# Kernel optimization log

Hardware: AMD Instinct MI355X
Metric: run time of the kernel (lower is better)

Reference implementation:

```python
import jax, jax.numpy as jnp
import numpy as np

EPS = 1e-8
TOP_K = 2


def _l2norm(v, axis=-1):
    # F.normalize: v / max(||v||_2, eps)
    n = jnp.sqrt(jnp.sum(v * v, axis=axis, keepdims=True))
    return v / jnp.maximum(n, EPS)


def setup_inputs() -> dict:
    key = jax.random.key(0)
    ks = jax.random.split(key, 5)
    B, S, D, F, E = 2, 2048, 512, 2048, 8
    x = jax.random.normal(ks[0], (B, S, D), dtype=jnp.float32)
    anchors = jax.random.normal(ks[1], (E, D), dtype=jnp.float32)
    W1 = jax.random.normal(ks[2], (E, D, F), dtype=jnp.float32) * (1.0 / np.sqrt(D))
    b1 = jnp.zeros((E, F), dtype=jnp.float32)
    W2 = jax.random.normal(ks[3], (E, F, D), dtype=jnp.float32) * (1.0 / np.sqrt(F))
    b2 = jnp.zeros((E, D), dtype=jnp.float32)
    return {"x": x, "anchors": anchors, "W1": W1, "b1": b1, "W2": W2, "b2": b2}


def reference(x, anchors, W1, b1, W2, b2):
    B, S, D = x.shape
    E = anchors.shape[0]
    x_flat = x.reshape(B * S, D)  # (T, D)

    # Semantic resonance routing: cosine similarity with anchors
    x_n = _l2norm(x_flat)
    a_n = _l2norm(anchors)
    scores = jnp.einsum('td,ed->te', x_n, a_n)  # (T, E)

    # Noisy top-k (eval mode: no noise) + softmax gates over top-k scores
    topk_scores, topk_idx = jax.lax.top_k(scores, TOP_K)  # (T, K)
    gates = jax.nn.softmax(topk_scores, axis=-1)  # (T, K)

    # Combine weights per (token, expert); top-k indices are distinct per token
    T = B * S
    combine = jnp.zeros((T, E), dtype=x.dtype)
    combine = combine.at[jnp.arange(T)[:, None], topk_idx].add(gates)

    # Per-expert MLP (Linear -> exact GELU -> Linear), combined by gates.
    # Dense-over-experts form is mathematically identical to the sorted
    # grouped dispatch + index_add in the original module.
    h = jnp.einsum('td,edf->tef', x_flat, W1) + b1[None]  # (T, E, F)
    h = jax.nn.gelu(h, approximate=False)
    y = jnp.einsum('tef,efd->ted', h, W2) + b2[None]  # (T, E, D)
    out_flat = jnp.einsum('te,ted->td', combine, y)  # (T, D)

    out = out_flat.reshape(B, S, D)
    # aux_data equivalents: anchors_norm, resonance_scores, topk_indices
    return out, a_n, scores, topk_idx
```

## Files before the change

### kernel.cpp

```cpp
#include <hip/hip_runtime.h>
#include <cstdint>


#define T_TOK 4096
#define D_DIM 512
#define F_DIM 2048
#define E_EXP 8
#define NROWS 9216
#define MAXTILES 72

typedef __bf16 bf16x8 __attribute__((ext_vector_type(8)));
typedef float  f32x4  __attribute__((ext_vector_type(4)));
typedef unsigned short u16;

__device__ __forceinline__ u16 f2b(float f) {
    return __builtin_bit_cast(unsigned short, (__bf16)f);
}
__device__ __forceinline__ void gload16(void* lds, const void* g) {
    __builtin_amdgcn_global_load_lds(
        (const __attribute__((address_space(1))) void*)g,
        (__attribute__((address_space(3))) void*)lds, 16, 0, 0);
}

__global__ void anchors_k(const float* __restrict__ anchors,
                          float* __restrict__ an, float* __restrict__ dout_an) {
    int tid = threadIdx.x;
    int lane = tid & 63, e = tid >> 6;
    const float4* ar = (const float4*)(anchors + e * D_DIM + lane * 8);
    float4 v0 = ar[0], v1 = ar[1];
    float ss = v0.x*v0.x + v0.y*v0.y + v0.z*v0.z + v0.w*v0.w
             + v1.x*v1.x + v1.y*v1.y + v1.z*v1.z + v1.w*v1.w;
#pragma unroll
    for (int off = 32; off >= 1; off >>= 1) ss += __shfl_xor(ss, off, 64);
    float inv = 1.0f / fmaxf(sqrtf(ss), 1e-8f);
    float o[8] = {v0.x*inv, v0.y*inv, v0.z*inv, v0.w*inv,
                  v1.x*inv, v1.y*inv, v1.z*inv, v1.w*inv};
#pragma unroll
    for (int i = 0; i < 8; ++i) {
        an[e * D_DIM + lane * 8 + i] = o[i];
        dout_an[e * D_DIM + lane * 8 + i] = o[i];
    }
}

__global__ void routing_k(const float* __restrict__ x, const float* __restrict__ an,
                          float* __restrict__ dout_scores, float* __restrict__ dout_idx,
                          int* __restrict__ idxs, float* __restrict__ gates,
                          int* __restrict__ cnt) {
    __shared__ float anl[E_EXP * 544];
    __shared__ int hist[E_EXP];
    int tid = threadIdx.x;
    if (tid < E_EXP) hist[tid] = 0;
    for (int i = tid; i < E_EXP * D_DIM; i += 256) {
        int e = i >> 9, d = i & 511;
        anl[e * 544 + (d >> 7) * 136 + (d & 127)] = an[i];
    }
    __syncthreads();

    int p = tid & 3;
    int tok = blockIdx.x * 64 + (tid >> 2);
    const float4* xr = (const float4*)(x + (size_t)tok * D_DIM + p * 128);
    const float* ab = &anl[p * 136];
    float dot[E_EXP] = {};
    float ss = 0.f;
    for (int c = 0; c < 32; ++c) {
        float4 xv = xr[c];
        ss += xv.x*xv.x + xv.y*xv.y + xv.z*xv.z + xv.w*xv.w;
#pragma unroll
        for (int e = 0; e < E_EXP; ++e) {
            float4 av = *(const float4*)&ab[e * 544 + c * 4];
            dot[e] += xv.x*av.x + xv.y*av.y + xv.z*av.z + xv.w*av.w;
        }
    }
#pragma unroll
    for (int off = 1; off <= 2; off <<= 1) {
        ss += __shfl_xor(ss, off, 64);
#pragma unroll
        for (int e = 0; e < E_EXP; ++e) dot[e] += __shfl_xor(dot[e], off, 64);
    }

    if (p == 0) {
        float inv = 1.0f / fmaxf(sqrtf(ss), 1e-8f);
        float s[E_EXP];
#pragma unroll
        for (int e = 0; e < E_EXP; ++e) s[e] = dot[e] * inv;
        int i0 = 0; float b0 = s[0];
#pragma unroll
        for (int e = 1; e < E_EXP; ++e) if (s[e] > b0) { b0 = s[e]; i0 = e; }
        int i1 = -1; float b1v = -1e30f;
#pragma unroll
        for (int e = 0; e < E_EXP; ++e)
            if (e != i0 && s[e] > b1v) { b1v = s[e]; i1 = e; }
        if (i1 < 0) { i1 = (i0 + 1) & 7; b1v = s[i1]; }
        float g0 = 1.0f / (1.0f + expf(b1v - b0));
        float g1 = 1.0f - g0;
#pragma unroll
        for (int e = 0; e < E_EXP; ++e) dout_scores[tok * E_EXP + e] = s[e];
        dout_idx[tok * 2 + 0] = (float)i0;
        dout_idx[tok * 2 + 1] = (float)i1;
        idxs[tok * 2 + 0] = i0; idxs[tok * 2 + 1] = i1;
        gates[tok * 2 + 0] = g0; gates[tok * 2 + 1] = g1;
        atomicAdd(&hist[i0], 1);
        atomicAdd(&hist[i1], 1);
    }
    __syncthreads();
    if (tid < E_EXP) atomicAdd(&cnt[tid], hist[tid]);
}

__global__ void offs_k(const int* __restrict__ cnt, int* __restrict__ offs,
                       int* __restrict__ cur) {
    if (threadIdx.x == 0 && blockIdx.x == 0) {
        int acc = 0;
        for (int e = 0; e < E_EXP; ++e) {
            offs[e] = acc; cur[e] = acc;
            acc += (cnt[e] + 127) & ~127;
        }
        offs[E_EXP] = acc;
    }
}

__global__ void assign_k(const int* __restrict__ idxs, const float* __restrict__ gates,
                         int* __restrict__ cur, int* __restrict__ rowmap,
                         float* __restrict__ rowgate) {
    int t = blockIdx.x * 256 + threadIdx.x;
    if (t >= T_TOK) return;
#pragma unroll
    for (int k = 0; k < 2; ++k) {
        int e = idxs[t * 2 + k];
        e = min(max(e, 0), E_EXP - 1);
        int r = atomicAdd(&cur[e], 1);
        if (r >= 0 && r < NROWS) {
            rowmap[r] = t;
            rowgate[r] = gates[t * 2 + k];
        }
    }
}

__global__ void gather_k(const float* __restrict__ x, const int* __restrict__ rowmap,
                         u16* __restrict__ Xg) {
    int r = blockIdx.x;
    int t = rowmap[r];
    int c = threadIdx.x * 2;
    ushort2 o;
    if (t < 0 || t >= T_TOK) { o.x = 0; o.y = 0; }
    else {
        float2 v = *(const float2*)(x + (size_t)t * D_DIM + c);
        o.x = f2b(v.x); o.y = f2b(v.y);
    }
    *(ushort2*)(Xg + (size_t)r * D_DIM + c) = o;
}

__global__ void transpose_cast_k(const float* __restrict__ in, u16* __restrict__ out,
                                 int R, int C) {
    size_t zoff = (size_t)blockIdx.z * R * C;
    in += zoff; out += zoff;
    __shared__ float t[32][33];
    int c0 = blockIdx.x * 32, r0 = blockIdx.y * 32;
    int tx = threadIdx.x, ty = threadIdx.y;
#pragma unroll
    for (int j = 0; j < 32; j += 8)
        t[ty + j][tx] = in[(size_t)(r0 + ty + j) * C + c0 + tx];
    __syncthreads();
#pragma unroll
    for (int j = 0; j < 32; j += 8)
        out[(size_t)(c0 + ty + j) * R + r0 + tx] = f2b(t[tx][ty + j]);
}

template <int MODE>
__launch_bounds__(256, 2)
__global__ void gemm_k(const u16* __restrict__ A, int lda,
                       const u16* __restrict__ BtBase, int ldb,
                       u16* __restrict__ Hout, const float* __restrict__ b1,
                       float* __restrict__ outacc,
                       const int* __restrict__ rowmap, const float* __restrict__ rowgate,
                       const int* __restrict__ offs, int kPer) {
    int row0 = blockIdx.y * 128;
    if (row0 >= offs[E_EXP]) return;
    int e = 0;
#pragma unroll
    for (int i = 1; i < E_EXP; ++i) if (row0 >= offs[i]) e = i;
    const u16* Bt = BtBase + (size_t)e * D_DIM * F_DIM;
    int n0 = blockIdx.x * 128;
    int k_begin = (MODE == 1) ? (int)blockIdx.z * kPer : 0;
    int k_end = k_begin + kPer;

    alignas(16) __shared__ u16 As[128 * 64];
    alignas(16) __shared__ u16 Bs[128 * 64];

    int tid = threadIdx.x;
    int lane = tid & 63;
    int wv = tid >> 6;
    int wm = wv & 1, wn = wv >> 1;
    int kq = lane >> 4;
    int l15 = lane & 15;

    const u16* aSrc[4]; const u16* bSrc[4];
    u16* aDst[4]; u16* bDst[4];
#pragma unroll
    for (int i = 0; i < 4; ++i) {
        int slot = i * 256 + tid;
        int m = slot >> 3;
        int kc = slot & 7;
        aSrc[i] = A + (size_t)(row0 + m) * lda + kc * 8;
        bSrc[i] = Bt + (size_t)(n0 + m) * ldb + kc * 8;
        aDst[i] = As + slot * 8;
        bDst[i] = Bs + slot * 8;
    }

    f32x4 acc[4][4];
#pragma unroll
    for (int i = 0; i < 4; ++i)
#pragma unroll
        for (int j = 0; j < 4; ++j) acc[i][j] = f32x4{0.f, 0.f, 0.f, 0.f};

    for (int k0 = k_begin; k0 < k_end; k0 += 64) {
#pragma unroll
        for (int i = 0; i < 4; ++i) gload16(aDst[i], aSrc[i] + k0);
#pragma unroll
        for (int i = 0; i < 4; ++i) gload16(bDst[i], bSrc[i] + k0);
        asm volatile("s_waitcnt vmcnt(0)" ::: "memory");
        __syncthreads();
#pragma unroll
        for (int kk = 0; kk < 2; ++kk) {
            int kc = kk * 4 + kq;
            bf16x8 af[4], bfr[4];
#pragma unroll
            for (int i = 0; i < 4; ++i) {
                int rowA = wm * 64 + i * 16 + l15;
                af[i] = *(const bf16x8*)(As + rowA * 64 + kc * 8);
                int rowB = wn * 64 + i * 16 + l15;
                bfr[i] = *(const bf16x8*)(Bs + rowB * 64 + kc * 8);
            }
#pragma unroll
            for (int i = 0; i < 4; ++i)
#pragma unroll
                for (int j = 0; j < 4; ++j)
                    acc[i][j] = __builtin_amdgcn_mfma_f32_16x16x32_bf16(
                        af[i], bfr[j], acc[i][j], 0, 0, 0);
        }
        __syncthreads();
    }

    if constexpr (MODE == 0) {
        const float* b1e = b1 + (size_t)e * F_DIM;
#pragma unroll
        for (int i = 0; i < 4; ++i) {
            int gr = row0 + wm * 64 + i * 16 + kq * 4;
#pragma unroll
            for (int j = 0; j < 4; ++j) {
                int gc = n0 + wn * 64 + j * 16 + l15;
                float bb = b1e[gc];
#pragma unroll
                for (int r = 0; r < 4; ++r) {
                    float v = acc[i][j][r] + bb;
                    float h = 0.5f * v * (1.0f + erff(v * 0.70710678118f));
                    Hout[(size_t)(gr + r) * F_DIM + gc] = f2b(h);
                }
            }
        }
    } else {
#pragma unroll
        for (int i = 0; i < 4; ++i) {
            int grb = row0 + wm * 64 + i * 16 + kq * 4;
#pragma unroll
            for (int r = 0; r < 4; ++r) {
                int tok = rowmap[grb + r];
                float g = rowgate[grb + r];
                if (tok >= 0 && tok < T_TOK) {
                    float* orow = outacc + (size_t)tok * D_DIM;
#pragma unroll
                    for (int j = 0; j < 4; ++j) {
                        int gc = n0 + wn * 64 + j * 16 + l15;
                        atomicAdd(orow + gc, g * acc[i][j][r]);
                    }
                }
            }
        }
    }
}

__global__ void final_k(const float* __restrict__ outacc, const int* __restrict__ idxs,
                        const float* __restrict__ gates, const float* __restrict__ b2,
                        float* __restrict__ dout) {
    int t = blockIdx.x;
    int i0 = min(max(idxs[t * 2], 0), E_EXP - 1);
    int i1 = min(max(idxs[t * 2 + 1], 0), E_EXP - 1);
    float g0 = gates[t * 2], g1 = gates[t * 2 + 1];
    int d = threadIdx.x * 2;
    float2 oa = *(const float2*)(outacc + (size_t)t * D_DIM + d);
    const float* p0 = b2 + (size_t)i0 * D_DIM + d;
    const float* p1 = b2 + (size_t)i1 * D_DIM + d;
    float2 o;
    o.x = oa.x + g0 * p0[0] + g1 * p1[0];
    o.y = oa.y + g0 * p0[1] + g1 * p1[1];
    *(float2*)(dout + (size_t)t * D_DIM + d) = o;
}

#define OFF_AN      0u
#define OFF_CNT     0x10000u
#define OFF_OFFS    0x10100u
#define OFF_CUR     0x10200u
#define OFF_IDX     0x20000u
#define OFF_GATE    0x28000u
#define OFF_ROWMAP  0x30000u
#define OFF_ROWGATE 0x40000u
#define OFF_OUTACC  0x50000u
#define OFF_XG      0x900000u
#define OFF_W1T     0x1200000u
#define OFF_W2T     0x2200000u
#define OFF_HG      0x3200000u

extern "C" void kernel_launch(void* const* d_in, const int* in_sizes, int n_in,
                              void* d_out, int out_size, void* d_ws, size_t ws_size,
                              hipStream_t stream) {
    const float* x       = (const float*)d_in[0];
    const float* anchors = (const float*)d_in[1];
    const float* W1      = (const float*)d_in[2];
    const float* b1      = (const float*)d_in[3];
    const float* W2      = (const float*)d_in[4];
    const float* b2      = (const float*)d_in[5];
    float* out = (float*)d_out;

    char* ws = (char*)d_ws;
    float* an      = (float*)(ws + OFF_AN);
    int*   cnt     = (int*)(ws + OFF_CNT);
    int*   offs    = (int*)(ws + OFF_OFFS);
    int*   cur     = (int*)(ws + OFF_CUR);
    int*   idxs    = (int*)(ws + OFF_IDX);
    float* gates   = (float*)(ws + OFF_GATE);
    int*   rowmap  = (int*)(ws + OFF_ROWMAP);
    float* rowgate = (float*)(ws + OFF_ROWGATE);
    float* outacc  = (float*)(ws + OFF_OUTACC);
    u16*   Xg      = (u16*)(ws + OFF_XG);
    u16*   W1T     = (u16*)(ws + OFF_W1T);
    u16*   W2T     = (u16*)(ws + OFF_W2T);
    u16*   Hg      = (u16*)(ws + OFF_HG);

    float* out_main   = out;
    float* out_an     = out + (size_t)T_TOK * D_DIM;
    float* out_scores = out_an + E_EXP * D_DIM;
    float* out_idx    = out_scores + (size_t)T_TOK * E_EXP;

    hipMemsetAsync(cnt, 0, E_EXP * sizeof(int), stream);
    hipMemsetAsync(rowmap, 0xFF, NROWS * sizeof(int), stream);
    hipMemsetAsync(rowgate, 0, NROWS * sizeof(float), stream);
    hipMemsetAsync(outacc, 0, (size_t)T_TOK * D_DIM * sizeof(float), stream);

    anchors_k<<<1, 512, 0, stream>>>(anchors, an, out_an);
    routing_k<<<T_TOK / 64, 256, 0, stream>>>(x, an, out_scores, out_idx,
                                              idxs, gates, cnt);
    offs_k<<<1, 64, 0, stream>>>(cnt, offs, cur);
    assign_k<<<T_TOK / 256, 256, 0, stream>>>(idxs, gates, cur, rowmap, rowgate);
    gather_k<<<NROWS, 256, 0, stream>>>(x, rowmap, Xg);
    transpose_cast_k<<<dim3(F_DIM / 32, D_DIM / 32, E_EXP), dim3(32, 8), 0, stream>>>(
        W1, W1T, D_DIM, F_DIM);
    transpose_cast_k<<<dim3(D_DIM / 32, F_DIM / 32, E_EXP), dim3(32, 8), 0, stream>>>(
        W2, W2T, F_DIM, D_DIM);
    gemm_k<0><<<dim3(F_DIM / 128, MAXTILES, 1), 256, 0, stream>>>(
        Xg, D_DIM, W1T, D_DIM, Hg, b1, nullptr, rowmap, nullptr, offs, D_DIM);
    gemm_k<1><<<dim3(D_DIM / 128, MAXTILES, 2), 256, 0, stream>>>(
        Hg, F_DIM, W2T, F_DIM, nullptr, nullptr, outacc, rowmap, rowgate,
        offs, F_DIM / 2);
    final_k<<<T_TOK, 256, 0, stream>>>(outacc, idxs, gates, b2, out_main);
}
```

Baseline: 288.1 us.

## Swizzle GEMM LDS tiles, vectorize weight transpose, fuse memsets into init kernel

```diff
diff --git a/kernel.cpp b/kernel.cpp
--- a/kernel.cpp
+++ b/kernel.cpp
@@ -20,6 +20,17 @@
     __builtin_amdgcn_global_load_lds(
         (const __attribute__((address_space(1))) void*)g,
         (__attribute__((address_space(3))) void*)lds, 16, 0, 0);
+}
+
+__global__ void init_k(int* __restrict__ cnt, int* __restrict__ rowmap,
+                       float* __restrict__ rowgate, float* __restrict__ outacc) {
+    int tid = blockIdx.x * 256 + threadIdx.x;
+    int nth = gridDim.x * 256;
+    if (tid < E_EXP) cnt[tid] = 0;
+    for (int i = tid; i < NROWS; i += nth) { rowmap[i] = -1; rowgate[i] = 0.f; }
+    float4* o4 = (float4*)outacc;
+    for (int i = tid; i < (T_TOK * D_DIM) / 4; i += nth)
+        o4[i] = float4{0.f, 0.f, 0.f, 0.f};
 }
 
 __global__ void anchors_k(const float* __restrict__ anchors,
@@ -153,16 +164,27 @@
                                  int R, int C) {
     size_t zoff = (size_t)blockIdx.z * R * C;
     in += zoff; out += zoff;
-    __shared__ float t[32][33];
-    int c0 = blockIdx.x * 32, r0 = blockIdx.y * 32;
-    int tx = threadIdx.x, ty = threadIdx.y;
-#pragma unroll
-    for (int j = 0; j < 32; j += 8)
-        t[ty + j][tx] = in[(size_t)(r0 + ty + j) * C + c0 + tx];
+    __shared__ float t[64][65];
+    int c0 = blockIdx.x * 64, r0 = blockIdx.y * 64;
+    int tid = threadIdx.x;
+    int cq = tid & 15, rb = tid >> 4;
+#pragma unroll
+    for (int pass = 0; pass < 4; ++pass) {
+        int rr = rb + pass * 16;
+        float4 v = *(const float4*)(in + (size_t)(r0 + rr) * C + c0 + cq * 4);
+        t[rr][cq * 4 + 0] = v.x; t[rr][cq * 4 + 1] = v.y;
+        t[rr][cq * 4 + 2] = v.z; t[rr][cq * 4 + 3] = v.w;
+    }
     __syncthreads();
-#pragma unroll
-    for (int j = 0; j < 32; j += 8)
-        out[(size_t)(c0 + ty + j) * R + r0 + tx] = f2b(t[tx][ty + j]);
+    int rg = tid & 15, cb = tid >> 4;
+#pragma unroll
+    for (int pass = 0; pass < 4; ++pass) {
+        int c = cb + pass * 16;
+        ushort4 o;
+        o.x = f2b(t[rg * 4 + 0][c]); o.y = f2b(t[rg * 4 + 1][c]);
+        o.z = f2b(t[rg * 4 + 2][c]); o.w = f2b(t[rg * 4 + 3][c]);
+        *(ushort4*)(out + (size_t)(c0 + c) * R + r0 + rg * 4) = o;
+    }
 }
 
 template <int MODE>
@@ -199,7 +221,7 @@
     for (int i = 0; i < 4; ++i) {
         int slot = i * 256 + tid;
         int m = slot >> 3;
-        int kc = slot & 7;
+        int kc = (slot & 7) ^ (m & 7);
         aSrc[i] = A + (size_t)(row0 + m) * lda + kc * 8;
         bSrc[i] = Bt + (size_t)(n0 + m) * ldb + kc * 8;
         aDst[i] = As + slot * 8;
@@ -226,9 +248,9 @@
 #pragma unroll
             for (int i = 0; i < 4; ++i) {
                 int rowA = wm * 64 + i * 16 + l15;
-                af[i] = *(const bf16x8*)(As + rowA * 64 + kc * 8);
+                af[i] = *(const bf16x8*)(As + rowA * 64 + ((kc ^ (rowA & 7)) * 8));
                 int rowB = wn * 64 + i * 16 + l15;
-                bfr[i] = *(const bf16x8*)(Bs + rowB * 64 + kc * 8);
+                bfr[i] = *(const bf16x8*)(Bs + rowB * 64 + ((kc ^ (rowB & 7)) * 8));
             }
 #pragma unroll
             for (int i = 0; i < 4; ++i)
@@ -340,20 +362,16 @@
     float* out_scores = out_an + E_EXP * D_DIM;
     float* out_idx    = out_scores + (size_t)T_TOK * E_EXP;
 
-    hipMemsetAsync(cnt, 0, E_EXP * sizeof(int), stream);
-    hipMemsetAsync(rowmap, 0xFF, NROWS * sizeof(int), stream);
-    hipMemsetAsync(rowgate, 0, NROWS * sizeof(float), stream);
-    hipMemsetAsync(outacc, 0, (size_t)T_TOK * D_DIM * sizeof(float), stream);
-
+    init_k<<<512, 256, 0, stream>>>(cnt, rowmap, rowgate, outacc);
     anchors_k<<<1, 512, 0, stream>>>(anchors, an, out_an);
     routing_k<<<T_TOK / 64, 256, 0, stream>>>(x, an, out_scores, out_idx,
                                               idxs, gates, cnt);
     offs_k<<<1, 64, 0, stream>>>(cnt, offs, cur);
     assign_k<<<T_TOK / 256, 256, 0, stream>>>(idxs, gates, cur, rowmap, rowgate);
     gather_k<<<NROWS, 256, 0, stream>>>(x, rowmap, Xg);
-    transpose_cast_k<<<dim3(F_DIM / 32, D_DIM / 32, E_EXP), dim3(32, 8), 0, stream>>>(
+    transpose_cast_k<<<dim3(F_DIM / 64, D_DIM / 64, E_EXP), 256, 0, stream>>>(
         W1, W1T, D_DIM, F_DIM);
-    transpose_cast_k<<<dim3(D_DIM / 32, F_DIM / 32, E_EXP), dim3(32, 8), 0, stream>>>(
+    transpose_cast_k<<<dim3(D_DIM / 64, F_DIM / 64, E_EXP), 256, 0, stream>>>(
         W2, W2T, F_DIM, D_DIM);
     gemm_k<0><<<dim3(F_DIM / 128, MAXTILES, 1), 256, 0, stream>>>(
         Xg, D_DIM, W1T, D_DIM, Hg, b1, nullptr, rowmap, nullptr, offs, D_DIM);
```

After: 277.8 us. -3.6%, faster.
